# Optimization experiments

Measured on AMD Instinct MI355X. Metric: run time of the kernel, lower is better.

Reference implementation:

```python
import jax, jax.numpy as jnp
import numpy as np

N_SRC = 50000
N_DST = 50000
E = 800000
D = 128
OUT = 128


def setup_inputs() -> dict:
    key = jax.random.key(0)
    k1, k2, k3, k4, k5, k6 = jax.random.split(key, 6)
    lim = 1.0 / np.sqrt(D)
    return {
        "x_src": jax.random.normal(k1, (N_SRC, D), dtype=jnp.float32),
        "x_dst": jax.random.normal(k2, (N_DST, D), dtype=jnp.float32),
        "edge_src": jax.random.randint(k3, (E,), 0, N_SRC, dtype=jnp.int64),
        "edge_dst": jax.random.randint(k4, (E,), 0, N_DST, dtype=jnp.int64),
        "num_dst": N_DST,
        # learned params (torch nn.Linear: y = x @ W.T + b), stored here as [in, out]
        "W_neigh": jax.random.uniform(k5, (D, OUT), jnp.float32, -lim, lim),
        "b_neigh": jnp.zeros((OUT,), jnp.float32),
        "W_self": jax.random.uniform(k6, (D, OUT), jnp.float32, -lim, lim),
        "b_self": jnp.zeros((OUT,), jnp.float32),
    }


def reference(x_src, x_dst, edge_src, edge_dst, num_dst, W_neigh, b_neigh, W_self, b_self):
    # gather source features per edge: [E, D]
    neigh_feats = x_src[edge_src]
    # scatter-mean onto destination nodes
    summed = jax.ops.segment_sum(neigh_feats, edge_dst, num_segments=num_dst)  # [num_dst, D]
    count = jax.ops.segment_sum(jnp.ones((edge_dst.shape[0], 1), x_src.dtype), edge_dst,
                                num_segments=num_dst)
    agg = summed / jnp.clip(count, 1.0)
    # dual linear + add
    return agg @ W_neigh + b_neigh + x_dst @ W_self + b_self
```

## Files before the change

kernel.cpp:

```cpp
#include <hip/hip_runtime.h>

#define D 128
#define TM 64
#define CBITS 7
#define CSIZE 128
#define MAXNB 512
#define CAPB 2560

typedef __attribute__((ext_vector_type(8))) short bf16x8;
typedef __attribute__((ext_vector_type(4))) float f32x4;


__device__ __forceinline__ unsigned short f32_to_bf16(float x) {
    unsigned u = __float_as_uint(x);
    u += 0x7FFFu + ((u >> 16) & 1u);
    return (unsigned short)(u >> 16);
}
__device__ __forceinline__ float bf16_to_f32(unsigned short h) {
    return __uint_as_float(((unsigned)h) << 16);
}

__global__ __launch_bounds__(256) void prep_kernel(
    const float* __restrict__ Wn, const float* __restrict__ Ws,
    unsigned short* __restrict__ Wtn, unsigned short* __restrict__ Wts,
    int* __restrict__ gcursor, int NB) {
    const int stride = gridDim.x * 256;
    for (int i = blockIdx.x * 256 + threadIdx.x; i < D * D; i += stride) {
        int n = i >> 7, k = i & (D - 1);
        Wtn[i] = f32_to_bf16(Wn[k * D + n]);
        Wts[i] = f32_to_bf16(Ws[k * D + n]);
    }
    for (int i = blockIdx.x * 256 + threadIdx.x; i < NB; i += stride)
        gcursor[i] = 0;
}

__global__ __launch_bounds__(256) void fused_part_gemm_kernel(
    const int* __restrict__ edge_src, const int* __restrict__ edge_dst,
    int* __restrict__ gcursor, int* __restrict__ packed, int E, int NB,
    const float* __restrict__ x_src, const float* __restrict__ x_dst,
    const unsigned short* __restrict__ Wtn, const unsigned short* __restrict__ Wts,
    const float* __restrict__ bn, const float* __restrict__ bs,
    unsigned short* __restrict__ y16, float* __restrict__ out,
    int M_SRC, int N, int nblk, int blkA, int pstride) {
    __shared__ __align__(16) char smem[TM * 136 * 2 + D * 136 * 2];
    const int t = threadIdx.x;
    const int idx = (int)blockIdx.x;

    const bool isPart = (idx % pstride == 0) && (idx / pstride < nblk);

    if (isPart) {
        const int pid = idx / pstride;
        int* lh    = (int*)smem;
        int* lbase = lh + MAXNB;
        for (int i = t; i < NB; i += 256) lh[i] = 0;
        __syncthreads();
        const int base = pid * 2048;
        int es[8], ed[8];
        #pragma unroll
        for (int i = 0; i < 8; ++i) {
            int e = base + t + i * 256;
            if (e < E) { es[i] = edge_src[e]; ed[i] = edge_dst[e]; }
            else ed[i] = -1;
        }
        #pragma unroll
        for (int i = 0; i < 8; ++i)
            if (ed[i] >= 0) atomicAdd(&lh[ed[i] >> CBITS], 1);
        __syncthreads();
        for (int i = t; i < NB; i += 256) {
            int v = lh[i];
            lbase[i] = v ? atomicAdd(&gcursor[i], v) : 0;
        }
        __syncthreads();
        for (int i = t; i < NB; i += 256) lh[i] = 0;
        __syncthreads();
        #pragma unroll
        for (int i = 0; i < 8; ++i) {
            if (ed[i] >= 0) {
                int bk = ed[i] >> CBITS;
                int pos = lbase[bk] + atomicAdd(&lh[bk], 1);
                if (pos < CAPB)
                    packed[(size_t)bk * CAPB + pos] =
                        (es[i] << CBITS) | (ed[i] & (CSIZE - 1));
            }
        }
        return;
    }

    typedef unsigned short ushort136[136];
    ushort136* LA = (ushort136*)smem;
    ushort136* LW = (ushort136*)(smem + TM * 136 * 2);

    const int npb  = min((idx + pstride - 1) / pstride, nblk);
    const int gb   = idx - npb;
    const bool isA  = gb < blkA;
    const int  row0 = (isA ? gb : gb - blkA) * TM;
    const int  M    = isA ? M_SRC : N;
    const float* Ap = isA ? x_src : x_dst;
    const unsigned short* Wp = isA ? Wtn : Wts;

    {
        const float4* Av = (const float4*)Ap;
        #pragma unroll
        for (int i = 0; i < 8; ++i) {
            int vi = t + i * 256;
            int r = vi >> 5, c4 = vi & 31;
            int sr = min(row0 + r, M - 1);
            float4 v = Av[(size_t)sr * 32 + c4];
            ushort4 p;
            p.x = f32_to_bf16(v.x); p.y = f32_to_bf16(v.y);
            p.z = f32_to_bf16(v.z); p.w = f32_to_bf16(v.w);
            *(ushort4*)&LA[r][c4 * 4] = p;
        }
        const int4* Wv = (const int4*)Wp;
        #pragma unroll
        for (int i = 0; i < 8; ++i) {
            int vi = t + i * 256;
            int r = vi >> 4, c8 = vi & 15;
            *(int4*)&LW[r][c8 * 8] = Wv[vi];
        }
    }
    __syncthreads();

    const int lane = t & 63;
    const int wv   = t >> 6;
    const int wr   = wv & 1;
    const int wc   = wv >> 1;
    const int lr   = lane & 15;
    const int g    = lane >> 4;

    f32x4 acc[2][4];
    #pragma unroll
    for (int i = 0; i < 2; ++i)
        #pragma unroll
        for (int j = 0; j < 4; ++j) acc[i][j] = (f32x4){0.f, 0.f, 0.f, 0.f};

    #pragma unroll
    for (int kt = 0; kt < 4; ++kt) {
        bf16x8 b0 = *(const bf16x8*)&LW[wc * 64 + 0 * 16 + lr][kt * 32 + g * 8];
        bf16x8 b1 = *(const bf16x8*)&LW[wc * 64 + 1 * 16 + lr][kt * 32 + g * 8];
        bf16x8 b2 = *(const bf16x8*)&LW[wc * 64 + 2 * 16 + lr][kt * 32 + g * 8];
        bf16x8 b3 = *(const bf16x8*)&LW[wc * 64 + 3 * 16 + lr][kt * 32 + g * 8];
        bf16x8 a0 = *(const bf16x8*)&LA[wr * 32 + lr][kt * 32 + g * 8];
        bf16x8 a1 = *(const bf16x8*)&LA[wr * 32 + 16 + lr][kt * 32 + g * 8];
        acc[0][0] = __builtin_amdgcn_mfma_f32_16x16x32_bf16(a0, b0, acc[0][0], 0, 0, 0);
        acc[0][1] = __builtin_amdgcn_mfma_f32_16x16x32_bf16(a0, b1, acc[0][1], 0, 0, 0);
        acc[0][2] = __builtin_amdgcn_mfma_f32_16x16x32_bf16(a0, b2, acc[0][2], 0, 0, 0);
        acc[0][3] = __builtin_amdgcn_mfma_f32_16x16x32_bf16(a0, b3, acc[0][3], 0, 0, 0);
        acc[1][0] = __builtin_amdgcn_mfma_f32_16x16x32_bf16(a1, b0, acc[1][0], 0, 0, 0);
        acc[1][1] = __builtin_amdgcn_mfma_f32_16x16x32_bf16(a1, b1, acc[1][1], 0, 0, 0);
        acc[1][2] = __builtin_amdgcn_mfma_f32_16x16x32_bf16(a1, b2, acc[1][2], 0, 0, 0);
        acc[1][3] = __builtin_amdgcn_mfma_f32_16x16x32_bf16(a1, b3, acc[1][3], 0, 0, 0);
    }

    if (isA) {
        #pragma unroll
        for (int i = 0; i < 2; ++i) {
            #pragma unroll
            for (int j = 0; j < 4; ++j) {
                int col = wc * 64 + j * 16 + lr;
                #pragma unroll
                for (int r = 0; r < 4; ++r) {
                    int row = row0 + wr * 32 + i * 16 + g * 4 + r;
                    if (row < M)
                        y16[(size_t)row * D + col] = f32_to_bf16(acc[i][j][r]);
                }
            }
        }
    } else {
        #pragma unroll
        for (int i = 0; i < 2; ++i) {
            #pragma unroll
            for (int j = 0; j < 4; ++j) {
                int col = wc * 64 + j * 16 + lr;
                float bias = bn[col] + bs[col];
                #pragma unroll
                for (int r = 0; r < 4; ++r) {
                    int row = row0 + wr * 32 + i * 16 + g * 4 + r;
                    if (row < M)
                        out[(size_t)row * D + col] = acc[i][j][r] + bias;
                }
            }
        }
    }
}

__global__ __launch_bounds__(256) void fine_kernel(
    const int* __restrict__ packed, const int* __restrict__ gcursor,
    int* __restrict__ off_beg, int* __restrict__ off_end,
    int* __restrict__ eidx, int N) {
    __shared__ int dcount[CSIZE];
    __shared__ int dbase[CSIZE];
    __shared__ int sbuf[CSIZE];
    const int b  = blockIdx.x;
    const int d0 = b << CBITS;
    const int beg = b * CAPB;
    const int cnt = min(gcursor[b], CAPB);
    const int t = threadIdx.x;
    if (t < CSIZE) dcount[t] = 0;
    __syncthreads();
    for (int i = t; i < cnt; i += 256)
        atomicAdd(&dcount[packed[beg + i] & (CSIZE - 1)], 1);
    __syncthreads();
    if (t < CSIZE) sbuf[t] = dcount[t];
    __syncthreads();
    for (int ofs = 1; ofs < CSIZE; ofs <<= 1) {
        int u = (t < CSIZE && t >= ofs) ? sbuf[t - ofs] : 0;
        __syncthreads();
        if (t < CSIZE) sbuf[t] += u;
        __syncthreads();
    }
    if (t < CSIZE) {
        int excl = sbuf[t] - dcount[t];
        dbase[t] = excl;
        int d = d0 + t;
        if (d < N) {
            off_beg[d] = beg + excl;
            off_end[d] = beg + excl + dcount[t];
        }
    }
    __syncthreads();
    if (t < CSIZE) dcount[t] = dbase[t];
    __syncthreads();
    for (int i = t; i < cnt; i += 256) {
        int p = packed[beg + i];
        int pos = beg + atomicAdd(&dcount[p & (CSIZE - 1)], 1);
        eidx[pos] = p >> CBITS;
    }
}

__global__ void gather_out_kernel(const unsigned short* __restrict__ y16,
                                  const int* __restrict__ off_beg,
                                  const int* __restrict__ off_end,
                                  const int* __restrict__ eidx,
                                  float* __restrict__ out, int N) {
    const int wave = (int)(((long long)blockIdx.x * blockDim.x + threadIdx.x) >> 6);
    const int lane = threadIdx.x & 63;
    if (wave >= N) return;
    const int h = lane >> 4;
    const int c = lane & 15;
    const int beg = off_beg[wave];
    const int end = off_end[wave];

    float acc[8];
    #pragma unroll
    for (int j = 0; j < 8; ++j) acc[j] = 0.f;

    for (int i = beg + h; i < end; i += 4) {
        int s = eidx[i];
        const int4 v = *reinterpret_cast<const int4*>(y16 + (size_t)s * D + c * 8);
        const unsigned short* hs = (const unsigned short*)&v;
        #pragma unroll
        for (int j = 0; j < 8; ++j) acc[j] += bf16_to_f32(hs[j]);
    }

    #pragma unroll
    for (int j = 0; j < 8; ++j) {
        acc[j] += __shfl_down(acc[j], 32);
        acc[j] += __shfl_down(acc[j], 16);
    }

    if (h == 0) {
        const float inv = 1.0f / fmaxf((float)(end - beg), 1.0f);
        float4* o = reinterpret_cast<float4*>(out + (size_t)wave * D) + c * 2;
        float4 c0 = o[0], c1 = o[1];
        c0.x = fmaf(acc[0], inv, c0.x);
        c0.y = fmaf(acc[1], inv, c0.y);
        c0.z = fmaf(acc[2], inv, c0.z);
        c0.w = fmaf(acc[3], inv, c0.w);
        c1.x = fmaf(acc[4], inv, c1.x);
        c1.y = fmaf(acc[5], inv, c1.y);
        c1.z = fmaf(acc[6], inv, c1.z);
        c1.w = fmaf(acc[7], inv, c1.w);
        o[0] = c0;
        o[1] = c1;
    }
}

extern "C" void kernel_launch(void* const* d_in, const int* in_sizes, int n_in,
                              void* d_out, int out_size, void* d_ws, size_t ws_size,
                              hipStream_t stream) {
    const float* x_src    = (const float*)d_in[0];
    const float* x_dst    = (const float*)d_in[1];
    const int*   edge_src = (const int*)d_in[2];
    const int*   edge_dst = (const int*)d_in[3];
    const float* Wn = (const float*)d_in[5];
    const float* bn = (const float*)d_in[6];
    const float* Ws = (const float*)d_in[7];
    const float* bs = (const float*)d_in[8];

    const int E     = in_sizes[2];
    const int N     = in_sizes[1] / D;
    const int M_SRC = in_sizes[0] / D;

    const int NB   = (N + CSIZE - 1) >> CBITS;
    const int nblk = (E + 2047) / 2048;

    unsigned short* y16 = (unsigned short*)d_ws;
    unsigned short* Wtn = y16 + (size_t)M_SRC * D;
    unsigned short* Wts = Wtn + D * D;
    int* packed  = (int*)(Wts + D * D);
    int* eidx    = packed + (size_t)NB * CAPB;
    int* off_beg = eidx + (size_t)NB * CAPB;
    int* off_end = off_beg + N;
    int* gcursor = off_end + N;

    const int T = 256;
    prep_kernel<<<32, T, 0, stream>>>(Wn, Ws, Wtn, Wts, gcursor, NB);

    const int blkA = (M_SRC + TM - 1) / TM;
    const int blkB = (N + TM - 1) / TM;
    const int total = nblk + blkA + blkB;
    const int pstride = total / nblk > 1 ? total / nblk : 1;
    fused_part_gemm_kernel<<<total, T, 0, stream>>>(
        edge_src, edge_dst, gcursor, packed, E, NB,
        x_src, x_dst, Wtn, Wts, bn, bs, y16, (float*)d_out,
        M_SRC, N, nblk, blkA, pstride);

    fine_kernel<<<NB, T, 0, stream>>>(packed, gcursor, off_beg, off_end, eidx, N);

    gather_out_kernel<<<(N + 3) / 4, T, 0, stream>>>(
        y16, off_beg, off_end, eidx, (float*)d_out, N);
}
```

Before: 77.79 us.

## Read GEMM weights from global memory, split fine-kernel histogram per wave

The GEMM blocks no longer stage the bf16 weight matrix in LDS. They load the B fragments directly from global memory (L2-resident), which roughly halves shared memory per block and removes the staging loop. The fine bucketing kernel now keeps per-wave histograms and per-wave base offsets, which cuts LDS atomic contention and drops one barrier. gather_out_kernel also gets launch bounds. The risk is extra global-load latency inside the MFMA loop.

```diff
diff --git a/kernel.cpp b/kernel.cpp
--- a/kernel.cpp
+++ b/kernel.cpp
@@ -42,7 +42,7 @@
     const float* __restrict__ bn, const float* __restrict__ bs,
     unsigned short* __restrict__ y16, float* __restrict__ out,
     int M_SRC, int N, int nblk, int blkA, int pstride) {
-    __shared__ __align__(16) char smem[TM * 136 * 2 + D * 136 * 2];
+    __shared__ __align__(16) char smem[TM * 136 * 2];
     const int t = threadIdx.x;
     const int idx = (int)blockIdx.x;
 
@@ -88,7 +88,6 @@
 
     typedef unsigned short ushort136[136];
     ushort136* LA = (ushort136*)smem;
-    ushort136* LW = (ushort136*)(smem + TM * 136 * 2);
 
     const int npb  = min((idx + pstride - 1) / pstride, nblk);
     const int gb   = idx - npb;
@@ -111,13 +110,6 @@
             p.z = f32_to_bf16(v.z); p.w = f32_to_bf16(v.w);
             *(ushort4*)&LA[r][c4 * 4] = p;
         }
-        const int4* Wv = (const int4*)Wp;
-        #pragma unroll
-        for (int i = 0; i < 8; ++i) {
-            int vi = t + i * 256;
-            int r = vi >> 4, c8 = vi & 15;
-            *(int4*)&LW[r][c8 * 8] = Wv[vi];
-        }
     }
     __syncthreads();
 
@@ -136,12 +128,13 @@
 
     #pragma unroll
     for (int kt = 0; kt < 4; ++kt) {
-        bf16x8 b0 = *(const bf16x8*)&LW[wc * 64 + 0 * 16 + lr][kt * 32 + g * 8];
-        bf16x8 b1 = *(const bf16x8*)&LW[wc * 64 + 1 * 16 + lr][kt * 32 + g * 8];
-        bf16x8 b2 = *(const bf16x8*)&LW[wc * 64 + 2 * 16 + lr][kt * 32 + g * 8];
-        bf16x8 b3 = *(const bf16x8*)&LW[wc * 64 + 3 * 16 + lr][kt * 32 + g * 8];
-        bf16x8 a0 = *(const bf16x8*)&LA[wr * 32 + lr][kt * 32 + g * 8];
-        bf16x8 a1 = *(const bf16x8*)&LA[wr * 32 + 16 + lr][kt * 32 + g * 8];
+        const int kk = kt * 32 + g * 8;
+        bf16x8 b0 = *(const bf16x8*)&Wp[(size_t)(wc * 64 + 0 * 16 + lr) * D + kk];
+        bf16x8 b1 = *(const bf16x8*)&Wp[(size_t)(wc * 64 + 1 * 16 + lr) * D + kk];
+        bf16x8 b2 = *(const bf16x8*)&Wp[(size_t)(wc * 64 + 2 * 16 + lr) * D + kk];
+        bf16x8 b3 = *(const bf16x8*)&Wp[(size_t)(wc * 64 + 3 * 16 + lr) * D + kk];
+        bf16x8 a0 = *(const bf16x8*)&LA[wr * 32 + lr][kk];
+        bf16x8 a1 = *(const bf16x8*)&LA[wr * 32 + 16 + lr][kk];
         acc[0][0] = __builtin_amdgcn_mfma_f32_16x16x32_bf16(a0, b0, acc[0][0], 0, 0, 0);
         acc[0][1] = __builtin_amdgcn_mfma_f32_16x16x32_bf16(a0, b1, acc[0][1], 0, 0, 0);
         acc[0][2] = __builtin_amdgcn_mfma_f32_16x16x32_bf16(a0, b2, acc[0][2], 0, 0, 0);
@@ -188,20 +181,29 @@
     const int* __restrict__ packed, const int* __restrict__ gcursor,
     int* __restrict__ off_beg, int* __restrict__ off_end,
     int* __restrict__ eidx, int N) {
-    __shared__ int dcount[CSIZE];
-    __shared__ int dbase[CSIZE];
+    __shared__ int dcount[4][CSIZE];
+    __shared__ int wbase[4][CSIZE];
     __shared__ int sbuf[CSIZE];
     const int b  = blockIdx.x;
     const int d0 = b << CBITS;
     const int beg = b * CAPB;
     const int cnt = min(gcursor[b], CAPB);
     const int t = threadIdx.x;
-    if (t < CSIZE) dcount[t] = 0;
+    const int wv = t >> 6;
+
+    if (t < CSIZE) {
+        dcount[0][t] = 0; dcount[1][t] = 0;
+        dcount[2][t] = 0; dcount[3][t] = 0;
+    }
     __syncthreads();
     for (int i = t; i < cnt; i += 256)
-        atomicAdd(&dcount[packed[beg + i] & (CSIZE - 1)], 1);
-    __syncthreads();
-    if (t < CSIZE) sbuf[t] = dcount[t];
+        atomicAdd(&dcount[wv][packed[beg + i] & (CSIZE - 1)], 1);
+    __syncthreads();
+    int tot = 0;
+    if (t < CSIZE) {
+        tot = dcount[0][t] + dcount[1][t] + dcount[2][t] + dcount[3][t];
+        sbuf[t] = tot;
+    }
     __syncthreads();
     for (int ofs = 1; ofs < CSIZE; ofs <<= 1) {
         int u = (t < CSIZE && t >= ofs) ? sbuf[t - ofs] : 0;
@@ -210,29 +212,33 @@
         __syncthreads();
     }
     if (t < CSIZE) {
-        int excl = sbuf[t] - dcount[t];
-        dbase[t] = excl;
+        int excl = sbuf[t] - tot;
         int d = d0 + t;
         if (d < N) {
             off_beg[d] = beg + excl;
-            off_end[d] = beg + excl + dcount[t];
-        }
-    }
-    __syncthreads();
-    if (t < CSIZE) dcount[t] = dbase[t];
+            off_end[d] = beg + excl + tot;
+        }
+        int run = excl;
+        #pragma unroll
+        for (int w = 0; w < 4; ++w) {
+            wbase[w][t] = run;
+            run += dcount[w][t];
+        }
+    }
     __syncthreads();
     for (int i = t; i < cnt; i += 256) {
         int p = packed[beg + i];
-        int pos = beg + atomicAdd(&dcount[p & (CSIZE - 1)], 1);
+        int pos = beg + atomicAdd(&wbase[wv][p & (CSIZE - 1)], 1);
         eidx[pos] = p >> CBITS;
     }
 }
 
-__global__ void gather_out_kernel(const unsigned short* __restrict__ y16,
-                                  const int* __restrict__ off_beg,
-                                  const int* __restrict__ off_end,
-                                  const int* __restrict__ eidx,
-                                  float* __restrict__ out, int N) {
+__global__ __launch_bounds__(256) void gather_out_kernel(
+    const unsigned short* __restrict__ y16,
+    const int* __restrict__ off_beg,
+    const int* __restrict__ off_end,
+    const int* __restrict__ eidx,
+    float* __restrict__ out, int N) {
     const int wave = (int)(((long long)blockIdx.x * blockDim.x + threadIdx.x) >> 6);
     const int lane = threadIdx.x & 63;
     if (wave >= N) return;
```

Result: slower. 81.71 us (+5.0%).
